# Kernel tuning notes

Measured on AMD Instinct MI355X. Metric: run time of the kernel, lower is better.

The kernel has to match this reference:

```python
import jax, jax.numpy as jnp
import numpy as np

B, T, HS = 2, 2048, 4096
H, HK, D = 32, 8, 128  # num_heads, num_kv_heads, head_dim; HS == H*D
N_REP = H // HK


def setup_inputs() -> dict:
    key = jax.random.key(0)
    k1, k2, k3 = jax.random.split(key, 3)
    x = jax.random.normal(k1, (B, T, HS), dtype=jnp.float32)
    # qkv Linear (no bias): out_features = HS + 2*HK*D
    W_qkv = jax.random.normal(k2, (HS + 2 * HK * D, HS), dtype=jnp.float32) * 0.02
    W_proj = jax.random.normal(k3, (HS, HS), dtype=jnp.float32) * 0.02
    # Realistic RoPE cache (rotate-half convention): [1, T, 1, D]
    pos = jnp.arange(T, dtype=jnp.float32)
    inv_freq = 1.0 / (10000.0 ** (jnp.arange(0, D, 2, dtype=jnp.float32) / D))
    ang = pos[:, None] * inv_freq[None, :]                      # [T, D/2]
    rope_cos = jnp.concatenate([jnp.cos(ang), jnp.cos(ang)], -1)[None, :, None, :]
    rope_sin = jnp.concatenate([jnp.sin(ang), jnp.sin(ang)], -1)[None, :, None, :]
    return {"x": x, "rope_cos": rope_cos, "rope_sin": rope_sin,
            "W_qkv": W_qkv, "W_proj": W_proj}


def _rotate_half(u):
    u1, u2 = jnp.split(u, 2, axis=-1)
    return jnp.concatenate([-u2, u1], axis=-1)


def _apply_rope(u, cos, sin):
    return u * cos + _rotate_half(u) * sin


def reference(x, rope_cos, rope_sin, W_qkv, W_proj):
    # fused QKV projection
    qkv = jnp.einsum('btc,oc->bto', x, W_qkv)
    q, k, v = jnp.split(qkv, [HS, HS + HK * D], axis=-1)
    q = q.reshape(B, T, H, D)
    k = k.reshape(B, T, HK, D)
    v = v.reshape(B, T, HK, D)
    # inline RoPE on q and k
    q = _apply_rope(q, rope_cos[:, :T], rope_sin[:, :T])
    k = _apply_rope(k, rope_cos[:, :T], rope_sin[:, :T])
    # GQA repeat_kv: [B,T,HK,D] -> [B,T,H,D]
    k = jnp.repeat(k, N_REP, axis=2)
    v = jnp.repeat(v, N_REP, axis=2)
    # causal attention (flash-equivalent math)
    scale = 1.0 / jnp.sqrt(jnp.asarray(D, dtype=q.dtype))
    scores = jnp.einsum('bqhd,bkhd->bhqk', q, k) * scale        # [B,H,T,T]
    causal = jnp.tril(jnp.ones((T, T), dtype=bool))
    scores = jnp.where(causal[None, None], scores, jnp.finfo(scores.dtype).min)
    p = jax.nn.softmax(scores, axis=-1)
    out = jnp.einsum('bhqk,bkhd->bqhd', p, v).reshape(B, T, HS)
    return jnp.einsum('btc,oc->bto', out, W_proj)
```

## Files before the change

kernel.cpp:

```cpp
#include <hip/hip_runtime.h>
#include <hip/hip_bf16.h>

typedef __attribute__((ext_vector_type(8))) short short8;
typedef __attribute__((ext_vector_type(4))) short short4v;
typedef __attribute__((ext_vector_type(4))) float floatx4;
typedef __attribute__((ext_vector_type(16))) float floatx16;
typedef __attribute__((ext_vector_type(4))) unsigned int uintx4;

__device__ __forceinline__ float b2f(ushort u) {
  unsigned x = ((unsigned)u) << 16;
  return __builtin_bit_cast(float, x);
}
__device__ __forceinline__ ushort f2b(float f) {
  unsigned x = __builtin_bit_cast(unsigned, f);
  x += 0x7fffu + ((x >> 16) & 1u);
  return (ushort)(x >> 16);
}

__device__ __forceinline__ void gload_lds16(const void* g, void* l) {
  __builtin_amdgcn_global_load_lds(
      (const __attribute__((address_space(1))) unsigned int*)g,
      (__attribute__((address_space(3))) unsigned int*)l, 16, 0, 0);
}

__device__ __forceinline__ short8 mkpa8(float p0, float p1, float p2, float p3,
                                        float p4, float p5, float p6, float p7) {
  unsigned a0, a1, b0, b1;
  asm("v_cvt_pk_bf16_f32 %0, %1, %2" : "=v"(a0) : "v"(p0), "v"(p1));
  asm("v_cvt_pk_bf16_f32 %0, %1, %2" : "=v"(a1) : "v"(p2), "v"(p3));
  asm("v_cvt_pk_bf16_f32 %0, %1, %2" : "=v"(b0) : "v"(p4), "v"(p5));
  asm("v_cvt_pk_bf16_f32 %0, %1, %2" : "=v"(b1) : "v"(p6), "v"(p7));
  asm volatile("v_permlane32_swap_b32 %0, %1" : "+v"(a0), "+v"(b0));
  asm volatile("v_permlane32_swap_b32 %0, %1" : "+v"(a1), "+v"(b1));
  uintx4 u;
  u[0] = a0;
  u[1] = a1;
  u[2] = b0;
  u[3] = b1;
  return __builtin_bit_cast(short8, u);
}

__global__ __launch_bounds__(256) void cvt_kernel(const float* __restrict__ in,
                                                  ushort* __restrict__ out, long n) {
  long i0 = ((long)blockIdx.x * 256 + threadIdx.x) * 4;
  long stride = (long)gridDim.x * 256 * 4;
  for (long i = i0; i < n; i += stride) {
    float4 v = *(const float4*)(in + i);
    ushort4 u;
    u.x = f2b(v.x); u.y = f2b(v.y); u.z = f2b(v.z); u.w = f2b(v.w);
    *(ushort4*)(out + i) = u;
  }
}

template <int BN, int OUTBF16>
__global__ __launch_bounds__(512, 2)
void gemm_pipe(const ushort* __restrict__ A, const ushort* __restrict__ B,
               float* __restrict__ Cf, ushort* __restrict__ Cb,
               int M, int N, int K) {
  constexpr int BNF = BN / 64;
  __shared__ __align__(16) ushort sA[2][256 * 64];
  __shared__ __align__(16) ushort sB[2][BN * 64];
  const int t = threadIdx.x;
  const int lane = t & 63;
  const int L = lane & 15, g = lane >> 4;
  const int w = t >> 6;
  const int wr = w >> 2, wc = w & 3;
  const int ntn = N / BN;
  const int nwg = gridDim.x;
  const int wg = blockIdx.x;
  const int swz = (wg & 7) * (nwg >> 3) + (wg >> 3);
  const int m0 = (swz / ntn) << 8;
  const int n0 = (swz % ntn) * BN;

  floatx4 acc[8][BNF];
#pragma unroll
  for (int i = 0; i < 8; i++)
#pragma unroll
    for (int j = 0; j < BNF; j++) acc[i][j] = (floatx4)(0.0f);

  const ushort* Ab = A + (size_t)m0 * K;
  const ushort* Bb = B + (size_t)n0 * K;

  auto stage_tile = [&](const ushort* Ag, const ushort* Bg, int buf) {
#pragma unroll
    for (int j = 0; j < 4; j++) {
      const int c = j * 512 + t;
      const int row = c >> 3, ch = c & 7;
      const int kc = ch ^ (row & 7);
      gload_lds16(Ag + (size_t)row * K + kc * 8, (char*)&sA[buf][0] + c * 16);
    }
#pragma unroll
    for (int j = 0; j < BN / 64; j++) {
      const int c = j * 512 + t;
      const int row = c >> 3, ch = c & 7;
      const int kc = ch ^ (row & 7);
      gload_lds16(Bg + (size_t)row * K + kc * 8, (char*)&sB[buf][0] + c * 16);
    }
  };
  auto rdA = [&](int buf, int mh, int kc16, short8* dst) {
#pragma unroll
    for (int i = 0; i < 4; i++) {
      const int row = wr * 128 + mh * 64 + i * 16 + L;
      const int ch = (kc16 * 4 + g) ^ (row & 7);
      dst[i] = *(const short8*)((const char*)&sA[buf][0] + row * 128 + ch * 16);
    }
  };
  auto rdB = [&](int buf, int kc16, short8* dst) {
#pragma unroll
    for (int i = 0; i < BNF; i++) {
      const int row = wc * (BN / 4) + i * 16 + L;
      const int ch = (kc16 * 4 + g) ^ (row & 7);
      dst[i] = *(const short8*)((const char*)&sB[buf][0] + row * 128 + ch * 16);
    }
  };

  short8 a0[4], a1[4], b0[BNF], b1[BNF];

  auto mfmaN = [&](short8* af, short8* bf, int accbase, int cnt) {
    __builtin_amdgcn_s_setprio(1);
    for (int i = 0; i < cnt; i++)
#pragma unroll
      for (int nf = 0; nf < BNF; nf++)
        acc[accbase + i][nf] =
            __builtin_amdgcn_mfma_f32_16x16x32_bf16(af[i], bf[nf], acc[accbase + i][nf], 0, 0, 0);
    __builtin_amdgcn_s_setprio(0);
  };

  const int NT = K >> 6;
  stage_tile(Ab, Bb, 0);
  __syncthreads();
  rdA(0, 0, 0, a0);
  rdB(0, 0, b0);

  for (int T = 0; T < NT; ++T) {
    const int p = T & 1, q = p ^ 1;
    const bool more = (T + 1 < NT);
    if (more) stage_tile(Ab + (T + 1) * 64, Bb + (T + 1) * 64, q);
    rdA(p, 1, 0, a1);
    mfmaN(a0, b0, 0, 4);
    rdA(p, 0, 1, a0);
    rdB(p, 1, b1);
    mfmaN(a1, b0, 4, 4);
    rdA(p, 1, 1, a1);
    mfmaN(a0, b1, 0, 4);
    mfmaN(a1, b1, 4, 2);
    __syncthreads();
    if (more) {
      rdA(q, 0, 0, a0);
      rdB(q, 0, b0);
    }
    mfmaN(a1 + 2, b1, 6, 2);
  }

#pragma unroll
  for (int mf = 0; mf < 8; mf++)
#pragma unroll
    for (int nf = 0; nf < BNF; nf++)
#pragma unroll
      for (int r = 0; r < 4; r++) {
        const int row = m0 + wr * 128 + mf * 16 + g * 4 + r;
        const int col = n0 + wc * (BN / 4) + nf * 16 + L;
        if (OUTBF16)
          Cb[(size_t)row * N + col] = f2b(acc[mf][nf][r]);
        else
          Cf[(size_t)row * N + col] = acc[mf][nf][r];
      }
}

__global__ __launch_bounds__(256)
void rope_kernel(const ushort* __restrict__ qkv, const float* __restrict__ cosp,
                 const float* __restrict__ sinp, ushort* __restrict__ Qo,
                 ushort* __restrict__ Ko) {
  const int row = blockIdx.x;
  const int b = row >> 11, tt = row & 2047;
  const int i = threadIdx.x;
  const ushort* qr = qkv + (size_t)row * 6144;

  const int jb = (i & 7) * 8;
  float cs[8], sn[8];
  *(float4*)&cs[0] = *(const float4*)(cosp + tt * 128 + jb);
  *(float4*)&cs[4] = *(const float4*)(cosp + tt * 128 + jb + 4);
  *(float4*)&sn[0] = *(const float4*)(sinp + tt * 128 + jb);
  *(float4*)&sn[4] = *(const float4*)(sinp + tt * 128 + jb + 4);

  {
    const int hh = i >> 3;
    short8 lo = *(const short8*)(qr + hh * 128 + jb);
    short8 hi = *(const short8*)(qr + hh * 128 + 64 + jb);
    short8 olo, ohi;
#pragma unroll
    for (int e = 0; e < 8; e++) {
      float fl = b2f((ushort)lo[e]), fh = b2f((ushort)hi[e]);
      olo[e] = (short)f2b(fl * cs[e] - fh * sn[e]);
      ohi[e] = (short)f2b(fh * cs[e] + fl * sn[e]);
    }
    ushort* dst = Qo + ((size_t)(b * 32 + hh) * 2048 + tt) * 128 + jb;
    *(short8*)dst = olo;
    *(short8*)(dst + 64) = ohi;
  }
  if (i < 64) {
    const int hkk = i >> 3;
    short8 lo = *(const short8*)(qr + 4096 + hkk * 128 + jb);
    short8 hi = *(const short8*)(qr + 4096 + hkk * 128 + 64 + jb);
    short8 olo, ohi;
#pragma unroll
    for (int e = 0; e < 8; e++) {
      float fl = b2f((ushort)lo[e]), fh = b2f((ushort)hi[e]);
      olo[e] = (short)f2b(fl * cs[e] - fh * sn[e]);
      ohi[e] = (short)f2b(fh * cs[e] + fl * sn[e]);
    }
    ushort* dst = Ko + ((size_t)(b * 8 + hkk) * 2048 + tt) * 128 + jb;
    *(short8*)dst = olo;
    *(short8*)(dst + 64) = ohi;
  }
}

__global__ __launch_bounds__(256)
void vtrans_kernel(const ushort* __restrict__ qkv, ushort* __restrict__ Vt) {
  const int bx = blockIdx.x;
  const int t0 = (bx & 31) * 64;
  const int hk = (bx >> 5) & 7;
  const int b = bx >> 8;
  const int i = threadIdx.x;
  const int tq = i & 15;
  const int dn = i >> 4;
  const ushort* src = qkv + ((size_t)(b * 2048 + t0 + tq * 4)) * 6144 + 5120 + hk * 128 + dn * 8;
  short8 v0 = *(const short8*)(src);
  short8 v1 = *(const short8*)(src + 6144);
  short8 v2 = *(const short8*)(src + 12288);
  short8 v3 = *(const short8*)(src + 18432);
  ushort* dst = Vt + ((size_t)(b * 8 + hk) * 128 + dn * 8) * 2048 + t0 + tq * 4;
#pragma unroll
  for (int e = 0; e < 8; e++) {
    short4v pk;
    pk[0] = v0[e]; pk[1] = v1[e]; pk[2] = v2[e]; pk[3] = v3[e];
    *(short4v*)(dst + (size_t)e * 2048) = pk;
  }
}

#define ATT_C2 0.1275172707611085f

__global__ __launch_bounds__(256, 2)
void attn_kernel(const ushort* __restrict__ Q, const ushort* __restrict__ Kg,
                 const ushort* __restrict__ Vtg, ushort* __restrict__ O) {
  __shared__ __align__(16) ushort Klds[2][64 * 128];
  __shared__ __align__(16) ushort Vlds[2][128 * 64];
  __shared__ __align__(16) ushort Olds[4][32 * 64];
  const int t = threadIdx.x, lane = t & 63, w = t >> 6;
  const int bx = blockIdx.x;
  const int hk = bx & 7;
  const int qh = (bx >> 3) & 3;
  const int b = (bx >> 5) & 1;
  const int pair = bx >> 6;
  const int h = hk * 4 + qh;
  const int qtA = pair, qtB = 15 - pair;
  const int nA = (qtA + 1) * 2, nB = (qtB + 1) * 2;
  const int total = nA + nB;

  const ushort* Qp = Q + ((size_t)(b * 32 + h) * 2048) * 128;
  const ushort* Kp = Kg + ((size_t)(b * 8 + hk) * 2048) * 128;
  const ushort* Vp = Vtg + ((size_t)(b * 8 + hk) * 128) * 2048;

  const int l31 = lane & 31;
  const int hi = lane >> 5;

  auto stage = [&](int s) {
    const int tt = (s < nA) ? s : s - nA;
    const int kv0 = tt * 64;
    ushort* Kd = Klds[s & 1];
    ushort* Vd = Vlds[s & 1];
#pragma unroll
    for (int j = 0; j < 4; j++) {
      const int c = j * 256 + t;
      const int krow = c >> 4, kcol = c & 15;
      gload_lds16(Kp + (size_t)(kv0 + krow) * 128 + ((kcol ^ (krow & 15)) << 3),
                  (char*)Kd + c * 16);
    }
#pragma unroll
    for (int j = 0; j < 4; j++) {
      const int c = j * 256 + t;
      const int d = c >> 3, tc = c & 7;
      gload_lds16(Vp + (size_t)d * 2048 + kv0 + ((tc ^ (d & 7)) << 3),
                  (char*)Vd + c * 16);
    }
  };

  short8 qf[8];
  floatx16 o[4];
  float mrun, lrun;

  auto init_pass = [&](int qw_) {
#pragma unroll
    for (int ks = 0; ks < 8; ks++)
      qf[ks] = *(const short8*)(Qp + (size_t)(qw_ + l31) * 128 + ks * 16 + hi * 8);
#pragma unroll
    for (int d = 0; d < 4; d++) o[d] = (floatx16)(0.0f);
    mrun = -3.0e38f;
    lrun = 0.0f;
  };

  auto compute = [&](int tt, int bsel, int qw_) {
    const int kv0 = tt * 64;
    if (kv0 > qw_ + 31) return;
    const ushort* Kd = Klds[bsel];
    const ushort* Vd = Vlds[bsel];
    floatx16 s0 = (floatx16)(0.0f), s1 = (floatx16)(0.0f);
    floatx16 s0x = (floatx16)(0.0f), s1x = (floatx16)(0.0f);
    __builtin_amdgcn_s_setprio(1);
#pragma unroll
    for (int ks = 0; ks < 8; ks += 2) {
      {
        const int gc = ks * 2 + hi;
        const int r0 = l31;
        short8 kf0 = *(const short8*)((const char*)Kd + r0 * 256 + ((gc ^ (r0 & 15)) * 16));
        s0 = __builtin_amdgcn_mfma_f32_32x32x16_bf16(kf0, qf[ks], s0, 0, 0, 0);
        const int r1 = 32 + l31;
        short8 kf1 = *(const short8*)((const char*)Kd + r1 * 256 + ((gc ^ (r1 & 15)) * 16));
        s1 = __builtin_amdgcn_mfma_f32_32x32x16_bf16(kf1, qf[ks], s1, 0, 0, 0);
      }
      {
        const int gc = (ks + 1) * 2 + hi;
        const int r0 = l31;
        short8 kf0 = *(const short8*)((const char*)Kd + r0 * 256 + ((gc ^ (r0 & 15)) * 16));
        s0x = __builtin_amdgcn_mfma_f32_32x32x16_bf16(kf0, qf[ks + 1], s0x, 0, 0, 0);
        const int r1 = 32 + l31;
        short8 kf1 = *(const short8*)((const char*)Kd + r1 * 256 + ((gc ^ (r1 & 15)) * 16));
        s1x = __builtin_amdgcn_mfma_f32_32x32x16_bf16(kf1, qf[ks + 1], s1x, 0, 0, 0);
      }
    }
    __builtin_amdgcn_s_setprio(0);
#pragma unroll
    for (int r = 0; r < 16; r++) { s0[r] += s0x[r]; s1[r] += s1x[r]; }
    const int qg = qw_ + l31;
    if (kv0 + 63 > qw_) {
#pragma unroll
      for (int r = 0; r < 16; r++) {
        const int kvr = (r & 3) + 8 * (r >> 2) + 4 * hi;
        if (kv0 + kvr > qg) s0[r] = -3.0e38f;
        if (kv0 + 32 + kvr > qg) s1[r] = -3.0e38f;
      }
    }
    float mm[16];
#pragma unroll
    for (int r = 0; r < 16; r++) mm[r] = fmaxf(s0[r], s1[r]);
#pragma unroll
    for (int st = 8; st > 0; st >>= 1)
#pragma unroll
      for (int r = 0; r < st; r++) mm[r] = fmaxf(mm[r], mm[r + st]);
    float m1 = fmaxf(mm[0], __shfl_xor(mm[0], 32, 64));
    if (!__all(m1 - mrun <= 62.73f)) {
      const float mnew = fmaxf(mrun, m1);
      const float alpha = __builtin_amdgcn_exp2f((mrun - mnew) * ATT_C2);
      lrun *= alpha;
#pragma unroll
      for (int d = 0; d < 4; d++)
#pragma unroll
        for (int r = 0; r < 16; r++) o[d][r] *= alpha;
      mrun = mnew;
    }
#pragma unroll
    for (int r = 0; r < 16; r++) {
      s0[r] = __builtin_amdgcn_exp2f((s0[r] - mrun) * ATT_C2);
      s1[r] = __builtin_amdgcn_exp2f((s1[r] - mrun) * ATT_C2);
    }
    float sm[16];
#pragma unroll
    for (int r = 0; r < 16; r++) sm[r] = s0[r] + s1[r];
#pragma unroll
    for (int st = 8; st > 0; st >>= 1)
#pragma unroll
      for (int r = 0; r < st; r++) sm[r] += sm[r + st];
    lrun += sm[0] + __shfl_xor(sm[0], 32, 64);
    short8 pa00 = mkpa8(s0[0], s0[1], s0[2], s0[3], s0[4], s0[5], s0[6], s0[7]);
    short8 pa01 = mkpa8(s0[8], s0[9], s0[10], s0[11], s0[12], s0[13], s0[14], s0[15]);
    short8 pa10 = mkpa8(s1[0], s1[1], s1[2], s1[3], s1[4], s1[5], s1[6], s1[7]);
    short8 pa11 = mkpa8(s1[8], s1[9], s1[10], s1[11], s1[12], s1[13], s1[14], s1[15]);
    __builtin_amdgcn_s_setprio(1);
#pragma unroll
    for (int kvb = 0; kvb < 2; kvb++)
#pragma unroll
      for (int sh = 0; sh < 2; sh++) {
        const short8 pa = (kvb == 0) ? (sh == 0 ? pa00 : pa01) : (sh == 0 ? pa10 : pa11);
        const int gc = kvb * 4 + sh * 2 + hi;
#pragma unroll
        for (int d = 0; d < 4; d++) {
          const int vr = d * 32 + l31;
          short8 vf = *(const short8*)((const char*)Vd + vr * 128 + ((gc ^ (vr & 7)) * 16));
          o[d] = __builtin_amdgcn_mfma_f32_32x32x16_bf16(vf, pa, o[d], 0, 0, 0);
        }
      }
    __builtin_amdgcn_s_setprio(0);
  };

  auto epilogue = [&](int qw_) {
    const float inv = 1.0f / lrun;
    ushort* Ow = Olds[w];
    const int q = l31;
#pragma unroll
    for (int half = 0; half < 2; half++) {
#pragma unroll
      for (int dd = 0; dd < 2; dd++) {
        const int dblk = half * 2 + dd;
#pragma unroll
        for (int rp = 0; rp < 8; rp++) {
          const int r0 = rp * 2;
          const int d0 = dd * 32 + (r0 & 3) + 8 * (r0 >> 2) + 4 * hi;
          unsigned pk;
          asm("v_cvt_pk_bf16_f32 %0, %1, %2" : "=v"(pk)
              : "v"(o[dblk][r0] * inv), "v"(o[dblk][r0 + 1] * inv));
          *(unsigned*)&Ow[q * 64 + (d0 ^ ((q & 7) << 3))] = pk;
        }
      }
#pragma unroll
      for (int qs = 0; qs < 4; qs++) {
        const int qq = qs * 8 + (lane >> 3);
        const int seg = lane & 7;
        short8 v = *(const short8*)&Ow[qq * 64 + ((seg * 8) ^ ((qq & 7) << 3))];
        *(short8*)&O[(size_t)(b * 2048 + qw_ + qq) * 4096 + h * 128 + half * 64 + seg * 8] = v;
      }
    }
  };

  int s = 0;
  stage(0);
  __syncthreads();

  int qw = qtA * 128 + w * 32;
  init_pass(qw);
  for (int i = 0; i < nA; ++i, ++s) {
    if (s + 1 < total) stage(s + 1);
    compute(i, s & 1, qw);
    __syncthreads();
  }
  epilogue(qw);

  qw = qtB * 128 + w * 32;
  init_pass(qw);
  for (int i = 0; i < nB; ++i, ++s) {
    if (s + 1 < total) stage(s + 1);
    compute(i, s & 1, qw);
    __syncthreads();
  }
  epilogue(qw);
}

extern "C" void kernel_launch(void* const* d_in, const int* in_sizes, int n_in,
                              void* d_out, int out_size, void* d_ws, size_t ws_size,
                              hipStream_t stream) {
  const float* x = (const float*)d_in[0];
  const float* rc = (const float*)d_in[1];
  const float* rs = (const float*)d_in[2];
  const float* wqkv = (const float*)d_in[3];
  const float* wproj = (const float*)d_in[4];
  float* out = (float*)d_out;

  ushort* xb = (ushort*)d_ws;
  ushort* wqkvb = xb + 16777216;
  ushort* qkvb = wqkvb + 25165824;
  ushort* Qb = qkvb + 25165824;
  ushort* Kb = Qb + 16777216;
  ushort* Vt = Kb + 4194304;
  ushort* wprojb = xb;
  ushort* aob = qkvb;

  cvt_kernel<<<2048, 256, 0, stream>>>(x, xb, 16777216L);
  cvt_kernel<<<2048, 256, 0, stream>>>(wqkv, wqkvb, 25165824L);
  gemm_pipe<192, 1><<<512, 512, 0, stream>>>(xb, wqkvb, nullptr, qkvb, 4096, 6144, 4096);
  rope_kernel<<<4096, 256, 0, stream>>>(qkvb, rc, rs, Qb, Kb);
  vtrans_kernel<<<512, 256, 0, stream>>>(qkvb, Vt);
  attn_kernel<<<512, 256, 0, stream>>>(Qb, Kb, Vt, aob);
  cvt_kernel<<<2048, 256, 0, stream>>>(wproj, wprojb, 16777216L);
  gemm_pipe<256, 0><<<256, 512, 0, stream>>>(aob, wprojb, out, nullptr, 4096, 4096, 4096);
}
```

Baseline: 474.9 us.

## Read K directly from global memory, one q-tile per block, more blocks

Drops the LDS staging of K tiles so that each wave loads K fragments straight from global memory, which frees LDS and raises the occupancy target to 3 blocks per CU. Replaces the paired light/heavy q-tile scheme with one q-tile per block and launches 1024 blocks, heaviest tiles first. It also removes the split dual-accumulator trick in the QK MFMA chain. In exchange, K reads are uncoalesced per-lane global loads that depend on cache hits, and causal load balance now relies on scheduling order rather than pairing.

```diff
diff --git a/kernel.cpp b/kernel.cpp
--- a/kernel.cpp
+++ b/kernel.cpp
@@ -240,10 +240,9 @@
 
 #define ATT_C2 0.1275172707611085f
 
-__global__ __launch_bounds__(256, 2)
+__global__ __launch_bounds__(256, 3)
 void attn_kernel(const ushort* __restrict__ Q, const ushort* __restrict__ Kg,
                  const ushort* __restrict__ Vtg, ushort* __restrict__ O) {
-  __shared__ __align__(16) ushort Klds[2][64 * 128];
   __shared__ __align__(16) ushort Vlds[2][128 * 64];
   __shared__ __align__(16) ushort Olds[4][32 * 64];
   const int t = threadIdx.x, lane = t & 63, w = t >> 6;
@@ -251,11 +250,9 @@
   const int hk = bx & 7;
   const int qh = (bx >> 3) & 3;
   const int b = (bx >> 5) & 1;
-  const int pair = bx >> 6;
+  const int qt = 15 - (bx >> 6);
   const int h = hk * 4 + qh;
-  const int qtA = pair, qtB = 15 - pair;
-  const int nA = (qtA + 1) * 2, nB = (qtB + 1) * 2;
-  const int total = nA + nB;
+  const int ntiles = (qt + 1) * 2;
 
   const ushort* Qp = Q + ((size_t)(b * 32 + h) * 2048) * 128;
   const ushort* Kp = Kg + ((size_t)(b * 8 + hk) * 2048) * 128;
@@ -263,19 +260,11 @@
 
   const int l31 = lane & 31;
   const int hi = lane >> 5;
-
-  auto stage = [&](int s) {
-    const int tt = (s < nA) ? s : s - nA;
-    const int kv0 = tt * 64;
-    ushort* Kd = Klds[s & 1];
+  const int qw = qt * 128 + w * 32;
+
+  auto stageV = [&](int s) {
+    const int kv0 = s * 64;
     ushort* Vd = Vlds[s & 1];
-#pragma unroll
-    for (int j = 0; j < 4; j++) {
-      const int c = j * 256 + t;
-      const int krow = c >> 4, kcol = c & 15;
-      gload_lds16(Kp + (size_t)(kv0 + krow) * 128 + ((kcol ^ (krow & 15)) << 3),
-                  (char*)Kd + c * 16);
-    }
 #pragma unroll
     for (int j = 0; j < 4; j++) {
       const int c = j * 256 + t;
@@ -287,52 +276,31 @@
 
   short8 qf[8];
   floatx16 o[4];
-  float mrun, lrun;
-
-  auto init_pass = [&](int qw_) {
-#pragma unroll
-    for (int ks = 0; ks < 8; ks++)
-      qf[ks] = *(const short8*)(Qp + (size_t)(qw_ + l31) * 128 + ks * 16 + hi * 8);
-#pragma unroll
-    for (int d = 0; d < 4; d++) o[d] = (floatx16)(0.0f);
-    mrun = -3.0e38f;
-    lrun = 0.0f;
-  };
-
-  auto compute = [&](int tt, int bsel, int qw_) {
+  float mrun = -3.0e38f, lrun = 0.0f;
+
+#pragma unroll
+  for (int ks = 0; ks < 8; ks++)
+    qf[ks] = *(const short8*)(Qp + (size_t)(qw + l31) * 128 + ks * 16 + hi * 8);
+#pragma unroll
+  for (int d = 0; d < 4; d++) o[d] = (floatx16)(0.0f);
+
+  auto compute = [&](int tt, int bsel) {
     const int kv0 = tt * 64;
-    if (kv0 > qw_ + 31) return;
-    const ushort* Kd = Klds[bsel];
+    if (kv0 > qw + 31) return;
     const ushort* Vd = Vlds[bsel];
+    const ushort* Kt = Kp + (size_t)kv0 * 128;
     floatx16 s0 = (floatx16)(0.0f), s1 = (floatx16)(0.0f);
-    floatx16 s0x = (floatx16)(0.0f), s1x = (floatx16)(0.0f);
     __builtin_amdgcn_s_setprio(1);
 #pragma unroll
-    for (int ks = 0; ks < 8; ks += 2) {
-      {
-        const int gc = ks * 2 + hi;
-        const int r0 = l31;
-        short8 kf0 = *(const short8*)((const char*)Kd + r0 * 256 + ((gc ^ (r0 & 15)) * 16));
-        s0 = __builtin_amdgcn_mfma_f32_32x32x16_bf16(kf0, qf[ks], s0, 0, 0, 0);
-        const int r1 = 32 + l31;
-        short8 kf1 = *(const short8*)((const char*)Kd + r1 * 256 + ((gc ^ (r1 & 15)) * 16));
-        s1 = __builtin_amdgcn_mfma_f32_32x32x16_bf16(kf1, qf[ks], s1, 0, 0, 0);
-      }
-      {
-        const int gc = (ks + 1) * 2 + hi;
-        const int r0 = l31;
-        short8 kf0 = *(const short8*)((const char*)Kd + r0 * 256 + ((gc ^ (r0 & 15)) * 16));
-        s0x = __builtin_amdgcn_mfma_f32_32x32x16_bf16(kf0, qf[ks + 1], s0x, 0, 0, 0);
-        const int r1 = 32 + l31;
-        short8 kf1 = *(const short8*)((const char*)Kd + r1 * 256 + ((gc ^ (r1 & 15)) * 16));
-        s1x = __builtin_amdgcn_mfma_f32_32x32x16_bf16(kf1, qf[ks + 1], s1x, 0, 0, 0);
-      }
+    for (int ks = 0; ks < 8; ks++) {
+      short8 kf0 = *(const short8*)(Kt + (size_t)l31 * 128 + ks * 16 + hi * 8);
+      s0 = __builtin_amdgcn_mfma_f32_32x32x16_bf16(kf0, qf[ks], s0, 0, 0, 0);
+      short8 kf1 = *(const short8*)(Kt + (size_t)(32 + l31) * 128 + ks * 16 + hi * 8);
+      s1 = __builtin_amdgcn_mfma_f32_32x32x16_bf16(kf1, qf[ks], s1, 0, 0, 0);
     }
     __builtin_amdgcn_s_setprio(0);
-#pragma unroll
-    for (int r = 0; r < 16; r++) { s0[r] += s0x[r]; s1[r] += s1x[r]; }
-    const int qg = qw_ + l31;
-    if (kv0 + 63 > qw_) {
+    const int qg = qw + l31;
+    if (kv0 + 63 > qw) {
 #pragma unroll
       for (int r = 0; r < 16; r++) {
         const int kvr = (r & 3) + 8 * (r >> 2) + 4 * hi;
@@ -392,7 +360,15 @@
     __builtin_amdgcn_s_setprio(0);
   };
 
-  auto epilogue = [&](int qw_) {
+  stageV(0);
+  __syncthreads();
+  for (int i = 0; i < ntiles; ++i) {
+    if (i + 1 < ntiles) stageV(i + 1);
+    compute(i, i & 1);
+    __syncthreads();
+  }
+
+  {
     const float inv = 1.0f / lrun;
     ushort* Ow = Olds[w];
     const int q = l31;
@@ -416,32 +392,10 @@
         const int qq = qs * 8 + (lane >> 3);
         const int seg = lane & 7;
         short8 v = *(const short8*)&Ow[qq * 64 + ((seg * 8) ^ ((qq & 7) << 3))];
-        *(short8*)&O[(size_t)(b * 2048 + qw_ + qq) * 4096 + h * 128 + half * 64 + seg * 8] = v;
+        *(short8*)&O[(size_t)(b * 2048 + qw + qq) * 4096 + h * 128 + half * 64 + seg * 8] = v;
       }
     }
-  };
-
-  int s = 0;
-  stage(0);
-  __syncthreads();
-
-  int qw = qtA * 128 + w * 32;
-  init_pass(qw);
-  for (int i = 0; i < nA; ++i, ++s) {
-    if (s + 1 < total) stage(s + 1);
-    compute(i, s & 1, qw);
-    __syncthreads();
-  }
-  epilogue(qw);
-
-  qw = qtB * 128 + w * 32;
-  init_pass(qw);
-  for (int i = 0; i < nB; ++i, ++s) {
-    if (s + 1 < total) stage(s + 1);
-    compute(i, s & 1, qw);
-    __syncthreads();
-  }
-  epilogue(qw);
+  }
 }
 
 extern "C" void kernel_launch(void* const* d_in, const int* in_sizes, int n_in,
@@ -468,7 +422,7 @@
   gemm_pipe<192, 1><<<512, 512, 0, stream>>>(xb, wqkvb, nullptr, qkvb, 4096, 6144, 4096);
   rope_kernel<<<4096, 256, 0, stream>>>(qkvb, rc, rs, Qb, Kb);
   vtrans_kernel<<<512, 256, 0, stream>>>(qkvb, Vt);
-  attn_kernel<<<512, 256, 0, stream>>>(Qb, Kb, Vt, aob);
+  attn_kernel<<<1024, 256, 0, stream>>>(Qb, Kb, Vt, aob);
   cvt_kernel<<<2048, 256, 0, stream>>>(wproj, wprojb, 16777216L);
   gemm_pipe<256, 0><<<256, 512, 0, stream>>>(aob, wprojb, out, nullptr, 4096, 4096, 4096);
 }
```

New measurement: 561.2 us. 1.18x slower.
